# Performance work log

Hardware: AMD Instinct MI355X
Metric: run time of the kernel (lower is better)

Reference implementation:

```python
import jax, jax.numpy as jnp
import numpy as np

N = 10000      # nodes
E = 160000     # directed edges
D_IN = 256     # node input feature dim
D_EIN = 128    # edge input feature dim
D = 256        # pretrans / hidden dim


def setup_inputs() -> dict:
    key = jax.random.key(0)
    ks = jax.random.split(key, 10)

    def w(k, shape):
        fan_in = shape[0]
        return jax.random.normal(k, shape, jnp.float32) * (1.0 / np.sqrt(fan_in))

    return {
        "x": jax.random.normal(ks[0], (N, D_IN), jnp.float32),
        "edge_feat": jax.random.normal(ks[1], (E, D_EIN), jnp.float32),
        "edge_index": jax.random.randint(ks[2], (2, E), 0, N),  # row0=src, row1=dst
        "Wn": w(ks[3], (D_IN, D)), "bn": jnp.zeros((D,), jnp.float32),
        "We": w(ks[4], (D_EIN, D)), "be": jnp.zeros((D,), jnp.float32),
        "Wpa": w(ks[5], (2 * D, D)), "bpa": jnp.zeros((D,), jnp.float32),
        "Wsa": w(ks[6], (2 * D, D)), "bsa": jnp.zeros((D,), jnp.float32),
        "Wnt": w(ks[7], (3 * D, D)), "bnt": jnp.zeros((D,), jnp.float32),
        "Wet": w(ks[8], (3 * D, D)), "bet": jnp.zeros((D,), jnp.float32),
    }


def reference(x, edge_feat, edge_index, Wn, bn, We, be, Wpa, bpa, Wsa, bsa, Wnt, bnt, Wet, bet):
    src, dst = edge_index[0], edge_index[1]

    # pretrans stage (per-node / per-edge MLPs)
    pre_n = jax.nn.relu(x @ Wn + bn)           # [N, D]
    pre_e = jax.nn.relu(edge_feat @ We + be)   # [E, D]

    ones = jnp.ones((pre_e.shape[0],), pre_n.dtype)
    deg_in = jax.ops.segment_sum(ones, dst, num_segments=N)   # predecessors per node
    deg_out = jax.ops.segment_sum(ones, src, num_segments=N)  # successors per node

    # predecessor aggregation at v: edges u->v, message = MLP(cat(pre_n[u], pre_e))
    msg_p = jax.nn.relu(jnp.concatenate([pre_n[src], pre_e], axis=-1) @ Wpa + bpa)  # [E, D]
    agg_p = jax.ops.segment_sum(msg_p, dst, num_segments=N) / jnp.maximum(deg_in, 1.0)[:, None]

    # successor aggregation at u: edges u->v, message = MLP(cat(pre_n[v], pre_e))
    msg_s = jax.nn.relu(jnp.concatenate([pre_n[dst], pre_e], axis=-1) @ Wsa + bsa)  # [E, D]
    agg_s = jax.ops.segment_sum(msg_s, src, num_segments=N) / jnp.maximum(deg_out, 1.0)[:, None]

    # node transformer on stack([pred_agg, self_pretrans, succ_agg]) -> flatten
    node_out = jnp.concatenate([agg_p, pre_n, agg_s], axis=-1) @ Wnt + bnt  # [N, D]

    # edge transformer on stack([src_pretrans, edge_pretrans, dst_pretrans])
    edge_out = jnp.concatenate([pre_n[src], pre_e, pre_n[dst]], axis=-1) @ Wet + bet  # [E, D]

    return node_out, edge_out
```

## Files before the change

### kernel.cpp

```cpp
#include <hip/hip_runtime.h>
#include <hip/hip_bf16.h>

#define N_NODES 10000
#define N_EDGES 160000
#define DD      256

typedef __bf16 bf16x8 __attribute__((ext_vector_type(8)));
typedef float  f32x4  __attribute__((ext_vector_type(4)));

__global__ void prep_weights_kernel(
    const float* __restrict__ Wn, const float* __restrict__ We,
    const float* __restrict__ Wnt, const float* __restrict__ Wpa,
    const float* __restrict__ Wsa, const float* __restrict__ Wet,
    __hip_bfloat16* __restrict__ Wn_t, __hip_bfloat16* __restrict__ We_t,
    __hip_bfloat16* __restrict__ Wnt_t, __hip_bfloat16* __restrict__ We_edge,
    __hip_bfloat16* __restrict__ Wn_node) {
  int idx = blockIdx.x * 256 + threadIdx.x;
  if (idx < 65536) {
    const int n = idx >> 8, k = idx & 255;
    Wn_t[idx] = __float2bfloat16(Wn[k * 256 + n]);
    return;
  }
  idx -= 65536;
  if (idx < 32768) {
    const int n = idx >> 7, k = idx & 127;
    We_t[idx] = __float2bfloat16(We[k * 256 + n]);
    return;
  }
  idx -= 32768;
  if (idx < 196608) {
    const int n = idx / 768, k = idx % 768;
    Wnt_t[idx] = __float2bfloat16(Wnt[k * 256 + n]);
    return;
  }
  idx -= 196608;
  if (idx < 196608) {
    const int n = idx >> 8, k = idx & 255;
    float v;
    if (n < 256)      v = Wpa[(256 + k) * 256 + n];
    else if (n < 512) v = Wsa[(256 + k) * 256 + (n - 256)];
    else              v = Wet[(256 + k) * 256 + (n - 512)];
    We_edge[idx] = __float2bfloat16(v);
    return;
  }
  idx -= 196608;
  if (idx < 262144) {
    const int n = idx >> 8, k = idx & 255;
    float v;
    if (n < 256)      v = Wpa[k * 256 + n];
    else if (n < 512) v = Wsa[k * 256 + (n - 256)];
    else if (n < 768) v = Wet[k * 256 + (n - 512)];
    else              v = Wet[(512 + k) * 256 + (n - 768)];
    Wn_node[idx] = __float2bfloat16(v);
  }
}

__global__ void count_kernel(const int* __restrict__ src, const int* __restrict__ dst,
                             int* __restrict__ cnt_out, int* __restrict__ cnt_in) {
  const int e = blockIdx.x * 256 + threadIdx.x;
  if (e < N_EDGES) {
    atomicAdd(&cnt_out[src[e]], 1);
    atomicAdd(&cnt_in[dst[e]], 1);
  }
}

__global__ __launch_bounds__(256) void scan2_kernel(
    const int* __restrict__ cnt_in, const int* __restrict__ cnt_out,
    int* __restrict__ offs_in, int* __restrict__ offs_out) {
  const int* cnt = blockIdx.x ? cnt_out : cnt_in;
  int* offs      = blockIdx.x ? offs_out : offs_in;
  const int n = N_NODES;
  __shared__ int part[256];
  const int t  = threadIdx.x;
  const int lo = t * 40;
  const int hi = (lo + 40 < n) ? lo + 40 : n;
  int s = 0;
  for (int i = lo; i < hi; ++i) s += cnt[i];
  part[t] = s;
  __syncthreads();
  for (int off = 1; off < 256; off <<= 1) {
    int v = (t >= off) ? part[t - off] : 0;
    __syncthreads();
    part[t] += v;
    __syncthreads();
  }
  int run = (t == 0) ? 0 : part[t - 1];
  for (int i = lo; i < hi; ++i) { offs[i] = run; run += cnt[i]; }
  if (t == 255) offs[n] = run;
}

__global__ void fill_kernel(const int* __restrict__ src, const int* __restrict__ dst,
                            const int* __restrict__ offs_out, const int* __restrict__ offs_in,
                            int* __restrict__ cur_out, int* __restrict__ cur_in,
                            int* __restrict__ pos_out, int* __restrict__ pos_in) {
  const int e = blockIdx.x * 256 + threadIdx.x;
  if (e < N_EDGES) {
    const int u = src[e];
    pos_out[e] = offs_out[u] + atomicAdd(&cur_out[u], 1);
    const int v = dst[e];
    pos_in[e] = offs_in[v] + atomicAdd(&cur_in[v], 1);
  }
}

template <bool RELU, bool F32OUT, bool A_F32>
__global__ __launch_bounds__(512, 4) void gemm_mfma_kernel(
    const void* __restrict__ Av, const __hip_bfloat16* __restrict__ Wt,
    const float* __restrict__ bias, float* __restrict__ outf,
    __hip_bfloat16* __restrict__ outb, int M, int Ksteps, int ldo) {
  __shared__ char sA[2][16384];
  __shared__ char sW[2][16384];

  const int K    = Ksteps * 64;
  const int row0 = blockIdx.x * 128;
  const int nt   = blockIdx.y;

  const int tid  = threadIdx.x;
  const int lane = tid & 63;
  const int w    = tid >> 6;

  const int rsub  = lane >> 3;
  const int pslot = lane & 7;
  const int sslot = pslot ^ rsub;

  auto stage = [&](int b, int c) {
#pragma unroll
    for (int j = 0; j < 2; ++j) {
      const int r = w * 16 + j * 8 + rsub;
      int ar = row0 + r;
      if (ar >= M) ar = M - 1;
      if constexpr (A_F32) {
        const float* gp = (const float*)Av + (size_t)ar * K + c * 64 + sslot * 8;
        const f32x4 lo = *(const f32x4*)gp;
        const f32x4 hi = *(const f32x4*)(gp + 4);
        union { __hip_bfloat16 h[8]; bf16x8 v; } pk;
#pragma unroll
        for (int q = 0; q < 4; ++q) pk.h[q] = __float2bfloat16(lo[q]);
#pragma unroll
        for (int q = 0; q < 4; ++q) pk.h[4 + q] = __float2bfloat16(hi[q]);
        *(bf16x8*)&sA[b][r * 128 + pslot * 16] = pk.v;
      } else {
        const __hip_bfloat16* gp =
            (const __hip_bfloat16*)Av + (size_t)ar * K + c * 64 + sslot * 8;
        __builtin_amdgcn_global_load_lds(
            (const __attribute__((address_space(1))) void*)gp,
            (__attribute__((address_space(3))) void*)&sA[b][(w * 16 + j * 8) * 128],
            16, 0, 0);
      }
      const __hip_bfloat16* wp = Wt + (size_t)(nt * 128 + r) * K + c * 64 + sslot * 8;
      __builtin_amdgcn_global_load_lds(
          (const __attribute__((address_space(1))) void*)wp,
          (__attribute__((address_space(3))) void*)&sW[b][(w * 16 + j * 8) * 128],
          16, 0, 0);
    }
  };

  const int wm = (w >> 1) * 32;
  const int wn = (w & 1) * 64;

  f32x4 acc[2][4];
#pragma unroll
  for (int i = 0; i < 2; ++i)
#pragma unroll
    for (int j = 0; j < 4; ++j) acc[i][j] = (f32x4)0.f;

  stage(0, 0);
  asm volatile("s_waitcnt vmcnt(0)");
  __syncthreads();

  int buf = 0;
  for (int c = 0; c < Ksteps; ++c) {
    if (c + 1 < Ksteps) stage(buf ^ 1, c + 1);
#pragma unroll
    for (int kk = 0; kk < 2; ++kk) {
      bf16x8 av[2], bv[4];
#pragma unroll
      for (int i = 0; i < 2; ++i) {
        const int row  = wm + i * 16 + (lane & 15);
        const int boff = row * 128 + ((kk * 64 + (lane >> 4) * 16) ^ ((row & 7) << 4));
        av[i] = *(const bf16x8*)&sA[buf][boff];
      }
#pragma unroll
      for (int j = 0; j < 4; ++j) {
        const int nrow = wn + j * 16 + (lane & 15);
        const int boff = nrow * 128 + ((kk * 64 + (lane >> 4) * 16) ^ ((nrow & 7) << 4));
        bv[j] = *(const bf16x8*)&sW[buf][boff];
      }
#pragma unroll
      for (int i = 0; i < 2; ++i)
#pragma unroll
        for (int j = 0; j < 4; ++j)
          acc[i][j] = __builtin_amdgcn_mfma_f32_16x16x32_bf16(av[i], bv[j], acc[i][j], 0, 0, 0);
    }
    __syncthreads();
    buf ^= 1;
  }

#pragma unroll
  for (int i = 0; i < 2; ++i) {
    const int row = row0 + wm + i * 16 + ((lane >> 4) << 2);
#pragma unroll
    for (int j = 0; j < 4; ++j) {
      const int col = nt * 128 + wn + j * 16 + (lane & 15);
      const float bb = bias ? bias[col] : 0.f;
#pragma unroll
      for (int r = 0; r < 4; ++r) {
        if (row + r < M) {
          float v = acc[i][j][r] + bb;
          if (RELU) v = v > 0.f ? v : 0.f;
          if (F32OUT) outf[(size_t)(row + r) * ldo + col] = v;
          else        outb[(size_t)(row + r) * ldo + col] = __float2bfloat16(v);
        }
      }
    }
  }
}

__global__ __launch_bounds__(512, 4) void pretrans_e_kernel(
    const float* __restrict__ ef, const __hip_bfloat16* __restrict__ We_t,
    const float* __restrict__ be, __hip_bfloat16* __restrict__ outb) {
  __shared__ char sA[2][16384];
  __shared__ char sW[2][16384];

  const int row0 = blockIdx.x * 128;
  const int tid  = threadIdx.x;
  const int lane = tid & 63;
  const int w    = tid >> 6;

  const int rsub  = lane >> 3;
  const int pslot = lane & 7;
  const int sslot = pslot ^ rsub;

  auto stageW = [&](int b, int t) {
    const int nt = t >> 1, c = t & 1;
#pragma unroll
    for (int j = 0; j < 2; ++j) {
      const int r = w * 16 + j * 8 + rsub;
      const __hip_bfloat16* wp = We_t + (size_t)(nt * 128 + r) * 128 + c * 64 + sslot * 8;
      __builtin_amdgcn_global_load_lds(
          (const __attribute__((address_space(1))) void*)wp,
          (__attribute__((address_space(3))) void*)&sW[b][(w * 16 + j * 8) * 128],
          16, 0, 0);
    }
  };

  stageW(0, 0);

#pragma unroll
  for (int c = 0; c < 2; ++c) {
#pragma unroll
    for (int j = 0; j < 2; ++j) {
      const int r = w * 16 + j * 8 + rsub;
      const float* gp = ef + (size_t)(row0 + r) * 128 + c * 64 + sslot * 8;
      const f32x4 lo = *(const f32x4*)gp;
      const f32x4 hi = *(const f32x4*)(gp + 4);
      union { __hip_bfloat16 h[8]; bf16x8 v; } pk;
#pragma unroll
      for (int q = 0; q < 4; ++q) pk.h[q] = __float2bfloat16(lo[q]);
#pragma unroll
      for (int q = 0; q < 4; ++q) pk.h[4 + q] = __float2bfloat16(hi[q]);
      *(bf16x8*)&sA[c][r * 128 + pslot * 16] = pk.v;
    }
  }

  const int wm = (w >> 1) * 32;
  const int wn = (w & 1) * 64;

  asm volatile("s_waitcnt vmcnt(0)");
  __syncthreads();

  int buf = 0;
  for (int nt = 0; nt < 2; ++nt) {
    f32x4 acc[2][4];
#pragma unroll
    for (int i = 0; i < 2; ++i)
#pragma unroll
      for (int j = 0; j < 4; ++j) acc[i][j] = (f32x4)0.f;

#pragma unroll
    for (int c = 0; c < 2; ++c) {
      const int t = nt * 2 + c;
      if (t + 1 < 4) stageW(buf ^ 1, t + 1);
#pragma unroll
      for (int kk = 0; kk < 2; ++kk) {
        bf16x8 av[2], bv[4];
#pragma unroll
        for (int i = 0; i < 2; ++i) {
          const int row  = wm + i * 16 + (lane & 15);
          const int boff = row * 128 + ((kk * 64 + (lane >> 4) * 16) ^ ((row & 7) << 4));
          av[i] = *(const bf16x8*)&sA[c][boff];
        }
#pragma unroll
        for (int j = 0; j < 4; ++j) {
          const int nrow = wn + j * 16 + (lane & 15);
          const int boff = nrow * 128 + ((kk * 64 + (lane >> 4) * 16) ^ ((nrow & 7) << 4));
          bv[j] = *(const bf16x8*)&sW[buf][boff];
        }
#pragma unroll
        for (int i = 0; i < 2; ++i)
#pragma unroll
          for (int j = 0; j < 4; ++j)
            acc[i][j] = __builtin_amdgcn_mfma_f32_16x16x32_bf16(av[i], bv[j], acc[i][j], 0, 0, 0);
      }
      __syncthreads();
      buf ^= 1;
    }

#pragma unroll
    for (int i = 0; i < 2; ++i) {
      const int row = row0 + wm + i * 16 + ((lane >> 4) << 2);
#pragma unroll
      for (int j = 0; j < 4; ++j) {
        const int col = nt * 128 + wn + j * 16 + (lane & 15);
        const float bb = be[col];
#pragma unroll
        for (int r = 0; r < 4; ++r) {
          float v = acc[i][j][r] + bb;
          v = v > 0.f ? v : 0.f;
          outb[(size_t)(row + r) * 256 + col] = __float2bfloat16(v);
        }
      }
    }
  }
}

template <bool MSG>
__global__ __launch_bounds__(512, 4) void edge_mfma_kernel(
    const __hip_bfloat16* __restrict__ pre_e,
    const __hip_bfloat16* __restrict__ We,
    const __hip_bfloat16* __restrict__ nodeP,
    const int* __restrict__ src, const int* __restrict__ dst,
    const int* __restrict__ pos_in, const int* __restrict__ pos_out,
    const float* __restrict__ bpa, const float* __restrict__ bsa,
    const float* __restrict__ bet,
    float* __restrict__ agg_p, float* __restrict__ agg_s,
    __hip_bfloat16* __restrict__ msg_p, __hip_bfloat16* __restrict__ msg_s,
    float* __restrict__ edge_out) {
  __shared__ char sA[4][8192];
  __shared__ char sW[2][16384];
  __shared__ int sSrc[64], sDst[64], sPin[64], sPout[64];

  const int et = blockIdx.x;
  const int e0 = et * 64;

  const int tid  = threadIdx.x;
  const int lane = tid & 63;
  const int w    = tid >> 6;

  if (tid < 64)        sSrc[tid] = src[e0 + tid];
  else if (tid < 128)  sDst[tid - 64] = dst[e0 + tid - 64];
  else if (tid < 192) { if (MSG) sPin[tid - 128]  = pos_in[e0 + tid - 128]; }
  else if (tid < 256) { if (MSG) sPout[tid - 192] = pos_out[e0 + tid - 192]; }

  const int rsub  = lane >> 3;
  const int pslot = lane & 7;
  const int sslot = pslot ^ rsub;

#pragma unroll
  for (int c = 0; c < 4; ++c) {
    const int r = w * 8 + rsub;
    const __hip_bfloat16* gp = pre_e + (size_t)(e0 + r) * 256 + c * 64 + sslot * 8;
    __builtin_amdgcn_global_load_lds(
        (const __attribute__((address_space(1))) void*)gp,
        (__attribute__((address_space(3))) void*)&sA[c][(w * 8) * 128],
        16, 0, 0);
  }

  auto stageW = [&](int b, int t) {
    const int nt = t >> 2, c = t & 3;
#pragma unroll
    for (int j = 0; j < 2; ++j) {
      const int r = w * 16 + j * 8 + rsub;
      const __hip_bfloat16* wp = We + (size_t)(nt * 128 + r) * 256 + c * 64 + sslot * 8;
      __builtin_amdgcn_global_load_lds(
          (const __attribute__((address_space(1))) void*)wp,
          (__attribute__((address_space(3))) void*)&sW[b][(w * 16 + j * 8) * 128],
          16, 0, 0);
    }
  };

  const int wm = (w >> 1) * 16;
  const int wn = (w & 1) * 64;

  stageW(0, 0);
  asm volatile("s_waitcnt vmcnt(0)");
  __syncthreads();

  int buf = 0;
  for (int nt = 0; nt < 6; ++nt) {
    const int mat = nt >> 1;
    f32x4 acc[4];
#pragma unroll
    for (int j = 0; j < 4; ++j) acc[j] = (f32x4)0.f;

#pragma unroll
    for (int c = 0; c < 4; ++c) {
      const int t = nt * 4 + c;
      if (t + 1 < 24) stageW(buf ^ 1, t + 1);
#pragma unroll
      for (int kk = 0; kk < 2; ++kk) {
        const int row  = wm + (lane & 15);
        const int aoff = row * 128 + ((kk * 64 + (lane >> 4) * 16) ^ ((row & 7) << 4));
        const bf16x8 av = *(const bf16x8*)&sA[c][aoff];
        bf16x8 bv[4];
#pragma unroll
        for (int j = 0; j < 4; ++j) {
          const int nrow = wn + j * 16 + (lane & 15);
          const int boff = nrow * 128 + ((kk * 64 + (lane >> 4) * 16) ^ ((nrow & 7) << 4));
          bv[j] = *(const bf16x8*)&sW[buf][boff];
        }
#pragma unroll
        for (int j = 0; j < 4; ++j)
          acc[j] = __builtin_amdgcn_mfma_f32_16x16x32_bf16(av, bv[j], acc[j], 0, 0, 0);
      }
      __syncthreads();
      buf ^= 1;
    }

    const int colbase = (nt & 1) * 128 + wn;
    const int lrow = wm + ((lane >> 4) << 2);
#pragma unroll
    for (int j = 0; j < 4; ++j) {
      const int col = colbase + j * 16 + (lane & 15);
      if (mat == 0) {
        const float bb = bpa[col];
#pragma unroll
        for (int r = 0; r < 4; ++r) {
          const int le = lrow + r;
          float v = acc[j][r] + bb +
                    __bfloat162float(nodeP[(size_t)sSrc[le] * 1024 + col]);
          v = v > 0.f ? v : 0.f;
          if (MSG) msg_p[(size_t)sPin[le] * 256 + col] = __float2bfloat16(v);
          else     atomicAdd(&agg_p[(size_t)sDst[le] * 256 + col], v);
        }
      } else if (mat == 1) {
        const float bb = bsa[col];
#pragma unroll
        for (int r = 0; r < 4; ++r) {
          const int le = lrow + r;
          float v = acc[j][r] + bb +
                    __bfloat162float(nodeP[(size_t)sDst[le] * 1024 + 256 + col]);
          v = v > 0.f ? v : 0.f;
          if (MSG) msg_s[(size_t)sPout[le] * 256 + col] = __float2bfloat16(v);
          else     atomicAdd(&agg_s[(size_t)sSrc[le] * 256 + col], v);
        }
      } else {
        const float bb = bet[col];
#pragma unroll
        for (int r = 0; r < 4; ++r) {
          const int le = lrow + r;
          float v = acc[j][r] + bb +
                    __bfloat162float(nodeP[(size_t)sSrc[le] * 1024 + 512 + col]) +
                    __bfloat162float(nodeP[(size_t)sDst[le] * 1024 + 768 + col]);
          edge_out[(size_t)(e0 + le) * 256 + col] = v;
        }
      }
    }
  }
}

__global__ __launch_bounds__(128) void agg_kernel(
    const __hip_bfloat16* __restrict__ msg_p, const __hip_bfloat16* __restrict__ msg_s,
    const __hip_bfloat16* __restrict__ pre_n,
    const int* __restrict__ offs_in, const int* __restrict__ offs_out,
    __hip_bfloat16* __restrict__ nodeH) {
  const int v    = blockIdx.x;
  const int wave = threadIdx.x >> 6;
  const int lane = threadIdx.x & 63;
  const int cg   = lane & 31;
  const int par  = lane >> 5;

  const int* offs = wave ? offs_out : offs_in;
  const __hip_bfloat16* msg = wave ? msg_s : msg_p;

  const int p0 = offs[v], p1 = offs[v + 1];
  float acc[8];
#pragma unroll
  for (int k = 0; k < 8; ++k) acc[k] = 0.f;

  for (int i = p0 + par; i < p1; i += 2) {
    const uint4 u = *(const uint4*)(msg + (size_t)i * 256 + cg * 8);
    const unsigned short* h = (const unsigned short*)&u;
#pragma unroll
    for (int k = 0; k < 8; ++k) acc[k] += __uint_as_float((unsigned)h[k] << 16);
  }
#pragma unroll
  for (int k = 0; k < 8; ++k) acc[k] += __shfl_xor(acc[k], 32);

  if (par == 0) {
    const int deg = p1 - p0;
    const float inv = 1.f / (float)(deg > 1 ? deg : 1);
    union { __hip_bfloat16 h[8]; uint4 u; } o;
#pragma unroll
    for (int k = 0; k < 8; ++k) o.h[k] = __float2bfloat16(acc[k] * inv);
    *(uint4*)(nodeH + (size_t)v * 768 + wave * 512 + cg * 8) = o.u;
  } else if (wave == 0) {
    const uint4 u = *(const uint4*)(pre_n + (size_t)v * 256 + cg * 8);
    *(uint4*)(nodeH + (size_t)v * 768 + 256 + cg * 8) = u;
  }
}

__global__ void node_prep_kernel(const float* __restrict__ agg_p,
                                 const float* __restrict__ agg_s,
                                 const __hip_bfloat16* __restrict__ pre_n,
                                 const int* __restrict__ cnt_in,
                                 const int* __restrict__ cnt_out,
                                 __hip_bfloat16* __restrict__ nodeH) {
  const int row = blockIdx.x;
  const int c   = threadIdx.x;
  const float di = (float)(cnt_in[row]  > 1 ? cnt_in[row]  : 1);
  const float dd = (float)(cnt_out[row] > 1 ? cnt_out[row] : 1);
  nodeH[(size_t)row * 768 + c]       = __float2bfloat16(agg_p[(size_t)row * 256 + c] / di);
  nodeH[(size_t)row * 768 + 256 + c] = pre_n[(size_t)row * 256 + c];
  nodeH[(size_t)row * 768 + 512 + c] = __float2bfloat16(agg_s[(size_t)row * 256 + c] / dd);
}

extern "C" void kernel_launch(void* const* d_in, const int* in_sizes, int n_in,
                              void* d_out, int out_size, void* d_ws, size_t ws_size,
                              hipStream_t stream) {
  const float* x         = (const float*)d_in[0];
  const float* edge_feat = (const float*)d_in[1];
  const int*   edge_idx  = (const int*)d_in[2];
  const float* Wn  = (const float*)d_in[3];
  const float* bn  = (const float*)d_in[4];
  const float* We  = (const float*)d_in[5];
  const float* be  = (const float*)d_in[6];
  const float* Wpa = (const float*)d_in[7];
  const float* bpa = (const float*)d_in[8];
  const float* Wsa = (const float*)d_in[9];
  const float* bsa = (const float*)d_in[10];
  const float* Wnt = (const float*)d_in[11];
  const float* bnt = (const float*)d_in[12];
  const float* Wet = (const float*)d_in[13];
  const float* bet = (const float*)d_in[14];

  const int* src = edge_idx;
  const int* dst = edge_idx + N_EDGES;

  float* node_out = (float*)d_out;
  float* edge_out = (float*)d_out + (size_t)N_NODES * DD;

  char* p = (char*)d_ws;
  auto alloc = [&](size_t bytes) -> void* {
    void* r = (void*)p;
    p += (bytes + 255) & ~(size_t)255;
    return r;
  };

  __hip_bfloat16* pre_n_bf = (__hip_bfloat16*)alloc((size_t)N_NODES * DD * 2);
  __hip_bfloat16* pre_e_bf = (__hip_bfloat16*)alloc((size_t)N_EDGES * DD * 2);
  __hip_bfloat16* nodeH    = (__hip_bfloat16*)alloc((size_t)N_NODES * 768 * 2);
  __hip_bfloat16* nodeP    = (__hip_bfloat16*)alloc((size_t)N_NODES * 1024 * 2);
  __hip_bfloat16* We_edge  = (__hip_bfloat16*)alloc((size_t)768 * 256 * 2);
  __hip_bfloat16* Wn_node  = (__hip_bfloat16*)alloc((size_t)1024 * 256 * 2);
  __hip_bfloat16* Wn_t     = (__hip_bfloat16*)alloc((size_t)256 * 256 * 2);
  __hip_bfloat16* We_t     = (__hip_bfloat16*)alloc((size_t)256 * 128 * 2);
  __hip_bfloat16* Wnt_t    = (__hip_bfloat16*)alloc((size_t)256 * 768 * 2);
  int* csr_zero = (int*)alloc(4 * (size_t)N_NODES * 4);
  int* cnt_in   = csr_zero;
  int* cnt_out  = csr_zero + N_NODES;
  int* cur_in   = csr_zero + 2 * N_NODES;
  int* cur_out  = csr_zero + 3 * N_NODES;
  int* offs_in  = (int*)alloc(((size_t)N_NODES + 1) * 4);
  int* offs_out = (int*)alloc(((size_t)N_NODES + 1) * 4);
  int* pos_in   = (int*)alloc((size_t)N_EDGES * 4);
  int* pos_out  = (int*)alloc((size_t)N_EDGES * 4);

  const size_t msg_bytes = (size_t)N_EDGES * DD * 2;
  const size_t base_used = (size_t)(p - (char*)d_ws);
  const bool msg_mode = ws_size >= base_used + 2 * msg_bytes + 512;

  __hip_bfloat16* msg_p = nullptr;
  __hip_bfloat16* msg_s = nullptr;
  float* agg_p = nullptr;
  float* agg_s = nullptr;
  if (msg_mode) {
    msg_p = (__hip_bfloat16*)alloc(msg_bytes);
    msg_s = (__hip_bfloat16*)alloc(msg_bytes);
  } else {
    agg_p = (float*)alloc((size_t)N_NODES * DD * 4);
    agg_s = (float*)alloc((size_t)N_NODES * DD * 4);
  }

  hipMemsetAsync(csr_zero, 0, 4 * (size_t)N_NODES * 4, stream);
  if (!msg_mode)
    hipMemsetAsync(agg_p, 0, 2 * (size_t)N_NODES * DD * 4, stream);

  prep_weights_kernel<<<(753664 + 255) / 256, 256, 0, stream>>>(
      Wn, We, Wnt, Wpa, Wsa, Wet, Wn_t, We_t, Wnt_t, We_edge, Wn_node);

  count_kernel<<<(N_EDGES + 255) / 256, 256, 0, stream>>>(src, dst, cnt_out, cnt_in);
  if (msg_mode) {
    scan2_kernel<<<2, 256, 0, stream>>>(cnt_in, cnt_out, offs_in, offs_out);
    fill_kernel<<<(N_EDGES + 255) / 256, 256, 0, stream>>>(
        src, dst, offs_out, offs_in, cur_out, cur_in, pos_out, pos_in);
  }

  {
    dim3 g((N_NODES + 127) / 128, 2);
    gemm_mfma_kernel<true, false, true><<<g, 512, 0, stream>>>(
        x, Wn_t, bn, nullptr, pre_n_bf, N_NODES, 4, 256);
  }
  pretrans_e_kernel<<<N_EDGES / 128, 512, 0, stream>>>(
      edge_feat, We_t, be, pre_e_bf);
  {
    dim3 g((N_NODES + 127) / 128, 8);
    gemm_mfma_kernel<false, false, false><<<g, 512, 0, stream>>>(
        pre_n_bf, Wn_node, nullptr, nullptr, nodeP, N_NODES, 4, 1024);
  }

  if (msg_mode) {
    edge_mfma_kernel<true><<<N_EDGES / 64, 512, 0, stream>>>(
        pre_e_bf, We_edge, nodeP, src, dst, pos_in, pos_out,
        bpa, bsa, bet, nullptr, nullptr, msg_p, msg_s, edge_out);
    agg_kernel<<<N_NODES, 128, 0, stream>>>(
        msg_p, msg_s, pre_n_bf, offs_in, offs_out, nodeH);
  } else {
    edge_mfma_kernel<false><<<N_EDGES / 64, 512, 0, stream>>>(
        pre_e_bf, We_edge, nodeP, src, dst, nullptr, nullptr,
        bpa, bsa, bet, agg_p, agg_s, nullptr, nullptr, edge_out);
    node_prep_kernel<<<N_NODES, 256, 0, stream>>>(
        agg_p, agg_s, pre_n_bf, cnt_in, cnt_out, nodeH);
  }

  {
    dim3 g((N_NODES + 127) / 128, 2);
    gemm_mfma_kernel<false, true, false><<<g, 512, 0, stream>>>(
        nodeH, Wnt_t, bnt, node_out, nullptr, N_NODES, 12, 256);
  }
}
```

Baseline: 375.8 us.

## Fuse edge pretrans GEMM into edge MFMA kernel to avoid pre_e round-trip

```diff
diff --git a/kernel.cpp b/kernel.cpp
--- a/kernel.cpp
+++ b/kernel.cpp
@@ -215,117 +215,11 @@
   }
 }
 
-__global__ __launch_bounds__(512, 4) void pretrans_e_kernel(
-    const float* __restrict__ ef, const __hip_bfloat16* __restrict__ We_t,
-    const float* __restrict__ be, __hip_bfloat16* __restrict__ outb) {
-  __shared__ char sA[2][16384];
-  __shared__ char sW[2][16384];
-
-  const int row0 = blockIdx.x * 128;
-  const int tid  = threadIdx.x;
-  const int lane = tid & 63;
-  const int w    = tid >> 6;
-
-  const int rsub  = lane >> 3;
-  const int pslot = lane & 7;
-  const int sslot = pslot ^ rsub;
-
-  auto stageW = [&](int b, int t) {
-    const int nt = t >> 1, c = t & 1;
-#pragma unroll
-    for (int j = 0; j < 2; ++j) {
-      const int r = w * 16 + j * 8 + rsub;
-      const __hip_bfloat16* wp = We_t + (size_t)(nt * 128 + r) * 128 + c * 64 + sslot * 8;
-      __builtin_amdgcn_global_load_lds(
-          (const __attribute__((address_space(1))) void*)wp,
-          (__attribute__((address_space(3))) void*)&sW[b][(w * 16 + j * 8) * 128],
-          16, 0, 0);
-    }
-  };
-
-  stageW(0, 0);
-
-#pragma unroll
-  for (int c = 0; c < 2; ++c) {
-#pragma unroll
-    for (int j = 0; j < 2; ++j) {
-      const int r = w * 16 + j * 8 + rsub;
-      const float* gp = ef + (size_t)(row0 + r) * 128 + c * 64 + sslot * 8;
-      const f32x4 lo = *(const f32x4*)gp;
-      const f32x4 hi = *(const f32x4*)(gp + 4);
-      union { __hip_bfloat16 h[8]; bf16x8 v; } pk;
-#pragma unroll
-      for (int q = 0; q < 4; ++q) pk.h[q] = __float2bfloat16(lo[q]);
-#pragma unroll
-      for (int q = 0; q < 4; ++q) pk.h[4 + q] = __float2bfloat16(hi[q]);
-      *(bf16x8*)&sA[c][r * 128 + pslot * 16] = pk.v;
-    }
-  }
-
-  const int wm = (w >> 1) * 32;
-  const int wn = (w & 1) * 64;
-
-  asm volatile("s_waitcnt vmcnt(0)");
-  __syncthreads();
-
-  int buf = 0;
-  for (int nt = 0; nt < 2; ++nt) {
-    f32x4 acc[2][4];
-#pragma unroll
-    for (int i = 0; i < 2; ++i)
-#pragma unroll
-      for (int j = 0; j < 4; ++j) acc[i][j] = (f32x4)0.f;
-
-#pragma unroll
-    for (int c = 0; c < 2; ++c) {
-      const int t = nt * 2 + c;
-      if (t + 1 < 4) stageW(buf ^ 1, t + 1);
-#pragma unroll
-      for (int kk = 0; kk < 2; ++kk) {
-        bf16x8 av[2], bv[4];
-#pragma unroll
-        for (int i = 0; i < 2; ++i) {
-          const int row  = wm + i * 16 + (lane & 15);
-          const int boff = row * 128 + ((kk * 64 + (lane >> 4) * 16) ^ ((row & 7) << 4));
-          av[i] = *(const bf16x8*)&sA[c][boff];
-        }
-#pragma unroll
-        for (int j = 0; j < 4; ++j) {
-          const int nrow = wn + j * 16 + (lane & 15);
-          const int boff = nrow * 128 + ((kk * 64 + (lane >> 4) * 16) ^ ((nrow & 7) << 4));
-          bv[j] = *(const bf16x8*)&sW[buf][boff];
-        }
-#pragma unroll
-        for (int i = 0; i < 2; ++i)
-#pragma unroll
-          for (int j = 0; j < 4; ++j)
-            acc[i][j] = __builtin_amdgcn_mfma_f32_16x16x32_bf16(av[i], bv[j], acc[i][j], 0, 0, 0);
-      }
-      __syncthreads();
-      buf ^= 1;
-    }
-
-#pragma unroll
-    for (int i = 0; i < 2; ++i) {
-      const int row = row0 + wm + i * 16 + ((lane >> 4) << 2);
-#pragma unroll
-      for (int j = 0; j < 4; ++j) {
-        const int col = nt * 128 + wn + j * 16 + (lane & 15);
-        const float bb = be[col];
-#pragma unroll
-        for (int r = 0; r < 4; ++r) {
-          float v = acc[i][j][r] + bb;
-          v = v > 0.f ? v : 0.f;
-          outb[(size_t)(row + r) * 256 + col] = __float2bfloat16(v);
-        }
-      }
-    }
-  }
-}
-
 template <bool MSG>
 __global__ __launch_bounds__(512, 4) void edge_mfma_kernel(
-    const __hip_bfloat16* __restrict__ pre_e,
+    const float* __restrict__ ef,
+    const __hip_bfloat16* __restrict__ We_t,
+    const float* __restrict__ be,
     const __hip_bfloat16* __restrict__ We,
     const __hip_bfloat16* __restrict__ nodeP,
     const int* __restrict__ src, const int* __restrict__ dst,
@@ -355,15 +249,44 @@
   const int pslot = lane & 7;
   const int sslot = pslot ^ rsub;
 
-#pragma unroll
-  for (int c = 0; c < 4; ++c) {
-    const int r = w * 8 + rsub;
-    const __hip_bfloat16* gp = pre_e + (size_t)(e0 + r) * 256 + c * 64 + sslot * 8;
-    __builtin_amdgcn_global_load_lds(
-        (const __attribute__((address_space(1))) void*)gp,
-        (__attribute__((address_space(3))) void*)&sA[c][(w * 8) * 128],
-        16, 0, 0);
-  }
+  const int wm = (w >> 1) * 16;
+  const int wn = (w & 1) * 64;
+
+  {
+    const int r  = tid >> 3;
+    const int s0 = tid & 7;
+#pragma unroll
+    for (int t = 0; t < 2; ++t) {
+      const int s  = s0 + t * 8;
+      const int kb = s >> 3;
+      const int ss = s & 7;
+      const float* gp = ef + (size_t)(e0 + r) * 128 + s * 8;
+      const f32x4 lo = *(const f32x4*)gp;
+      const f32x4 hi = *(const f32x4*)(gp + 4);
+      union { __hip_bfloat16 h[8]; bf16x8 v; } pk;
+#pragma unroll
+      for (int q = 0; q < 4; ++q) pk.h[q] = __float2bfloat16(lo[q]);
+#pragma unroll
+      for (int q = 0; q < 4; ++q) pk.h[4 + q] = __float2bfloat16(hi[q]);
+      *(bf16x8*)&sA[kb][r * 128 + ((ss * 16) ^ ((r & 7) << 4))] = pk.v;
+    }
+  }
+
+  auto stageWt = [&](int h) {
+#pragma unroll
+    for (int j = 0; j < 2; ++j) {
+      const int r = w * 16 + j * 8 + rsub;
+#pragma unroll
+      for (int kb = 0; kb < 2; ++kb) {
+        const __hip_bfloat16* gp =
+            We_t + (size_t)(h * 128 + r) * 128 + kb * 64 + sslot * 8;
+        __builtin_amdgcn_global_load_lds(
+            (const __attribute__((address_space(1))) void*)gp,
+            (__attribute__((address_space(3))) void*)&sW[kb][(w * 16 + j * 8) * 128],
+            16, 0, 0);
+      }
+    }
+  };
 
   auto stageW = [&](int b, int t) {
     const int nt = t >> 2, c = t & 3;
@@ -378,10 +301,76 @@
     }
   };
 
-  const int wm = (w >> 1) * 16;
-  const int wn = (w & 1) * 64;
+  f32x4 accA0[4], accA1[4];
+#pragma unroll
+  for (int j = 0; j < 4; ++j) { accA0[j] = (f32x4)0.f; accA1[j] = (f32x4)0.f; }
+
+  stageWt(0);
+  asm volatile("s_waitcnt vmcnt(0)");
+  __syncthreads();
+
+#pragma unroll
+  for (int kb = 0; kb < 2; ++kb) {
+#pragma unroll
+    for (int kk = 0; kk < 2; ++kk) {
+      const int row  = wm + (lane & 15);
+      const int aoff = row * 128 + ((kk * 64 + (lane >> 4) * 16) ^ ((row & 7) << 4));
+      const bf16x8 av = *(const bf16x8*)&sA[kb][aoff];
+#pragma unroll
+      for (int j = 0; j < 4; ++j) {
+        const int nrow = wn + j * 16 + (lane & 15);
+        const int boff = nrow * 128 + ((kk * 64 + (lane >> 4) * 16) ^ ((nrow & 7) << 4));
+        const bf16x8 bv = *(const bf16x8*)&sW[kb][boff];
+        accA0[j] = __builtin_amdgcn_mfma_f32_16x16x32_bf16(av, bv, accA0[j], 0, 0, 0);
+      }
+    }
+  }
+  __syncthreads();
+  stageWt(1);
+  asm volatile("s_waitcnt vmcnt(0)");
+  __syncthreads();
+#pragma unroll
+  for (int kb = 0; kb < 2; ++kb) {
+#pragma unroll
+    for (int kk = 0; kk < 2; ++kk) {
+      const int row  = wm + (lane & 15);
+      const int aoff = row * 128 + ((kk * 64 + (lane >> 4) * 16) ^ ((row & 7) << 4));
+      const bf16x8 av = *(const bf16x8*)&sA[kb][aoff];
+#pragma unroll
+      for (int j = 0; j < 4; ++j) {
+        const int nrow = wn + j * 16 + (lane & 15);
+        const int boff = nrow * 128 + ((kk * 64 + (lane >> 4) * 16) ^ ((nrow & 7) << 4));
+        const bf16x8 bv = *(const bf16x8*)&sW[kb][boff];
+        accA1[j] = __builtin_amdgcn_mfma_f32_16x16x32_bf16(av, bv, accA1[j], 0, 0, 0);
+      }
+    }
+  }
+  __syncthreads();
 
   stageW(0, 0);
+
+  {
+    const int rowb = wm + ((lane >> 4) << 2);
+#pragma unroll
+    for (int h = 0; h < 2; ++h) {
+#pragma unroll
+      for (int j = 0; j < 4; ++j) {
+        const int col  = h * 128 + wn + j * 16 + (lane & 15);
+        const float bb = be[col];
+        const int c    = col >> 6;
+        const int cb2  = (col & 63) * 2;
+#pragma unroll
+        for (int r = 0; r < 4; ++r) {
+          const int row = rowb + r;
+          float v = (h == 0 ? accA0[j][r] : accA1[j][r]) + bb;
+          v = v > 0.f ? v : 0.f;
+          *(__hip_bfloat16*)&sA[c][row * 128 + (cb2 ^ ((row & 7) << 4))] =
+              __float2bfloat16(v);
+        }
+      }
+    }
+  }
+
   asm volatile("s_waitcnt vmcnt(0)");
   __syncthreads();
 
@@ -547,7 +536,6 @@
   };
 
   __hip_bfloat16* pre_n_bf = (__hip_bfloat16*)alloc((size_t)N_NODES * DD * 2);
-  __hip_bfloat16* pre_e_bf = (__hip_bfloat16*)alloc((size_t)N_EDGES * DD * 2);
   __hip_bfloat16* nodeH    = (__hip_bfloat16*)alloc((size_t)N_NODES * 768 * 2);
   __hip_bfloat16* nodeP    = (__hip_bfloat16*)alloc((size_t)N_NODES * 1024 * 2);
   __hip_bfloat16* We_edge  = (__hip_bfloat16*)alloc((size_t)768 * 256 * 2);
@@ -600,8 +588,6 @@
     gemm_mfma_kernel<true, false, true><<<g, 512, 0, stream>>>(
         x, Wn_t, bn, nullptr, pre_n_bf, N_NODES, 4, 256);
   }
-  pretrans_e_kernel<<<N_EDGES / 128, 512, 0, stream>>>(
-      edge_feat, We_t, be, pre_e_bf);
   {
     dim3 g((N_NODES + 127) / 128, 8);
     gemm_mfma_kernel<false, false, false><<<g, 512, 0, stream>>>(
@@ -610,13 +596,13 @@
 
   if (msg_mode) {
     edge_mfma_kernel<true><<<N_EDGES / 64, 512, 0, stream>>>(
-        pre_e_bf, We_edge, nodeP, src, dst, pos_in, pos_out,
+        edge_feat, We_t, be, We_edge, nodeP, src, dst, pos_in, pos_out,
         bpa, bsa, bet, nullptr, nullptr, msg_p, msg_s, edge_out);
     agg_kernel<<<N_NODES, 128, 0, stream>>>(
         msg_p, msg_s, pre_n_bf, offs_in, offs_out, nodeH);
   } else {
     edge_mfma_kernel<false><<<N_EDGES / 64, 512, 0, stream>>>(
-        pre_e_bf, We_edge, nodeP, src, dst, nullptr, nullptr,
+        edge_feat, We_t, be, We_edge, nodeP, src, dst, nullptr, nullptr,
         bpa, bsa, bet, agg_p, agg_s, nullptr, nullptr, edge_out);
     node_prep_kernel<<<N_NODES, 256, 0, stream>>>(
         agg_p, agg_s, pre_n_bf, cnt_in, cnt_out, nodeH);
```

Measured after the change: 345.5 us. 1.09x faster.
